# Kernel tuning notes

Measured on AMD Instinct MI355X. Metric: run time of the kernel, lower is better.

## Reference

```python
import jax, jax.numpy as jnp
import numpy as np

L, E, H, FF = 6, 768, 4, 3072
D = E // H
SCALE = float(E) ** -0.5  # note: source scales by embedding_size**-0.5, not head_dim
EPS = 1e-5


def layernorm(x, scale, bias):
    mu = jnp.mean(x, axis=-1, keepdims=True)
    var = jnp.mean((x - mu) ** 2, axis=-1, keepdims=True)
    return (x - mu) * jax.lax.rsqrt(var + EPS) * scale + bias


def setup_inputs() -> dict:
    key = jax.random.key(0)
    ks = jax.random.split(key, 16)
    s = 0.02
    inp = {
        "hidden_states": jax.random.normal(ks[0], (8, 1024, E), dtype=jnp.float32),
        "ln1_scale": jnp.ones((L, E), jnp.float32),
        "ln1_bias": jnp.zeros((L, E), jnp.float32),
        "wq": jax.random.normal(ks[1], (L, E, E), jnp.float32) * s,
        "wk": jax.random.normal(ks[2], (L, E, E), jnp.float32) * s,
        "wv": jax.random.normal(ks[3], (L, E, E), jnp.float32) * s,
        "wo": jax.random.normal(ks[4], (L, E, E), jnp.float32) * s,
        "bo": jnp.zeros((L, E), jnp.float32),
        "ln2_scale": jnp.ones((L, E), jnp.float32),
        "ln2_bias": jnp.zeros((L, E), jnp.float32),
        "w1": jax.random.normal(ks[5], (L, FF, E), jnp.float32) * s,
        "b1": jnp.zeros((L, FF), jnp.float32),
        "w2": jax.random.normal(ks[6], (L, E, FF), jnp.float32) * s,
        "b2": jnp.zeros((L, E), jnp.float32),
    }
    return inp


def _encoder(x, ln1_scale, ln1_bias, wq, wk, wv, wo, bo, ln2_scale, ln2_bias, w1, b1, w2, b2):
    B, S, _ = x.shape
    for i in range(L):
        h = layernorm(x, ln1_scale[i], ln1_bias[i])
        # torch Linear: y = x @ W.T
        q = (h @ wq[i].T).reshape(B, H, S, D)  # non-standard head split (reshape, no transpose) per source
        k = (h @ wk[i].T).reshape(B, H, S, D)
        v = (h @ wv[i].T).reshape(B, H, S, D)
        scores = jnp.einsum("bhsd,bhtd->bhst", q, k) * SCALE  # full SxS materialized, as in source
        attn = jax.nn.softmax(scores, axis=-1)
        o = jnp.einsum("bhst,bhtd->bhsd", attn, v)
        o = o.transpose(0, 2, 1, 3).reshape(B, S, E)
        x = x + (o @ wo[i].T + bo[i])
        h = layernorm(x, ln2_scale[i], ln2_bias[i])
        h = jax.nn.gelu(h @ w1[i].T + b1[i], approximate=False)  # nn.GELU default = exact erf
        x = x + (h @ w2[i].T + b2[i])  # dropout is identity in eval
    return x


def reference(hidden_states, ln1_scale, ln1_bias, wq, wk, wv, wo, bo, ln2_scale, ln2_bias, w1, b1, w2, b2):
    return _encoder(hidden_states, ln1_scale, ln1_bias, wq, wk, wv, wo, bo, ln2_scale, ln2_bias, w1, b1, w2, b2)
```

## Files before the change

kernel.cpp:

```cpp
#include <hip/hip_runtime.h>
#include <math.h>

typedef __attribute__((ext_vector_type(8))) __bf16 bf16x8;
typedef __attribute__((ext_vector_type(4))) __bf16 bf16x4;
typedef __attribute__((ext_vector_type(2))) __bf16 bf16x2;
typedef __attribute__((ext_vector_type(4))) float f32x4;

#define MFMA_BF16 __builtin_amdgcn_mfma_f32_16x16x32_bf16

constexpr int LAY = 6, E = 768, HH = 4, DH = 192, FF = 3072, BB = 8, SS = 1024, MM = 8192;
constexpr float ATT_SCALE = 0.03608439182435161f;

__device__ __forceinline__ void gl2lds16(const void* g, void* l) {
    __builtin_amdgcn_global_load_lds(
        (const __attribute__((address_space(1))) void*)g,
        (__attribute__((address_space(3))) void*)l, 16, 0, 0);
}

struct Cast6 {
    const float* src[6];
    __bf16* dst[6];
    int cum4[7];
};

__global__ __launch_bounds__(256) void cast6_kernel(Cast6 c, int total4) {
    int stride = gridDim.x * 256;
    for (int i = blockIdx.x * 256 + threadIdx.x; i < total4; i += stride) {
        int rgn = 0;
#pragma unroll
        for (int k = 1; k < 6; ++k) rgn += (i >= c.cum4[k]) ? 1 : 0;
        int off = i - c.cum4[rgn];
        f32x4 v = ((const f32x4*)c.src[rgn])[off];
        bf16x4 o;
        o[0] = (__bf16)v[0]; o[1] = (__bf16)v[1]; o[2] = (__bf16)v[2]; o[3] = (__bf16)v[3];
        ((bf16x4*)c.dst[rgn])[off] = o;
    }
}

__global__ __launch_bounds__(256) void ln_kernel(const float* __restrict__ x,
                                                 const float* __restrict__ gamma,
                                                 const float* __restrict__ beta,
                                                 __bf16* __restrict__ out) {
    size_t row = blockIdx.x;
    const float* xr = x + row * E;
    int t = threadIdx.x;
    float v0 = xr[t], v1 = xr[t + 256], v2 = xr[t + 512];
    float s = v0 + v1 + v2;
    float q = v0 * v0 + v1 * v1 + v2 * v2;
#pragma unroll
    for (int m = 1; m < 64; m <<= 1) { s += __shfl_xor(s, m); q += __shfl_xor(q, m); }
    __shared__ float red[8];
    int w = t >> 6;
    if ((t & 63) == 0) { red[w] = s; red[4 + w] = q; }
    __syncthreads();
    s = red[0] + red[1] + red[2] + red[3];
    q = red[4] + red[5] + red[6] + red[7];
    float mu = s * (1.0f / E);
    float var = q * (1.0f / E) - mu * mu;
    float rs = rsqrtf(var + 1e-5f);
    __bf16* orow = out + row * E;
    orow[t]       = (__bf16)((v0 - mu) * rs * gamma[t]       + beta[t]);
    orow[t + 256] = (__bf16)((v1 - mu) * rs * gamma[t + 256] + beta[t + 256]);
    orow[t + 512] = (__bf16)((v2 - mu) * rs * gamma[t + 512] + beta[t + 512]);
}

template <int EPI>
__global__ __launch_bounds__(256, 2) void gemm128(
    const __bf16* __restrict__ A,
    const __bf16* __restrict__ B0, const __bf16* __restrict__ B1, const __bf16* __restrict__ B2,
    void* __restrict__ O0, void* __restrict__ O1, void* __restrict__ O2,
    const float* __restrict__ bias, int M, int N, int K) {
    __shared__ __bf16 lds[4 * 8192];
    int z = blockIdx.z;
    const __bf16* Bw = (z == 0) ? B0 : (z == 1) ? B1 : B2;
    void* Out = (z == 0) ? O0 : (z == 1) ? O1 : O2;
    int t = threadIdx.x;
    int w = t >> 6, lane = t & 63, b4 = lane >> 4, r = lane & 15;
    int gx = gridDim.x;
    int nwg = gx * gridDim.y;
    int bid = blockIdx.y * gx + blockIdx.x;
    int cpx = nwg >> 3;
    int swz = (bid & 7) * cpx + (bid >> 3);
    int bx = swz % gx, by = swz / gx;
    int mbase = by * 128, nbase = bx * 128;
    int wr = w >> 1, wc = w & 1;
    const f32x4 fz = {0.f, 0.f, 0.f, 0.f};
    f32x4 acc[4][4];
#pragma unroll
    for (int a1 = 0; a1 < 4; ++a1)
#pragma unroll
        for (int a2 = 0; a2 < 4; ++a2) acc[a1][a2] = fz;
    const __bf16* Ap = A + (size_t)mbase * K;
    const __bf16* Bp = Bw + (size_t)nbase * K;
    int nk = K >> 5;

    auto stage = [&](const __bf16* P, int regionB, int tt) {
        int base = (tt & 3) * 8192 + regionB * 4096;
#pragma unroll
        for (int i = 0; i < 2; ++i) {
            int c = i * 256 + t;
            int row = c >> 2, cl = c & 3;
            int sc = cl ^ ((row >> 1) & 3);
            gl2lds16(P + (size_t)row * K + tt * 32 + sc * 8,
                     (void*)(lds + base + (i * 256 + w * 64) * 8));
        }
    };
    int swch = (b4 ^ ((r >> 1) & 3)) * 8;
    int aoff = (wr * 64 + r) * 32 + swch;
    int boff = 4096 + (wc * 64 + r) * 32 + swch;

    stage(Ap, 0, 0); stage(Bp, 1, 0); stage(Ap, 0, 1);
    stage(Bp, 1, 1); stage(Ap, 0, 2); stage(Bp, 1, 2);

    for (int tt = 0; tt < nk; ++tt) {
        if (tt < nk - 2)       asm volatile("s_waitcnt vmcnt(8)" ::: "memory");
        else if (tt == nk - 2) asm volatile("s_waitcnt vmcnt(4)" ::: "memory");
        else                   asm volatile("s_waitcnt vmcnt(0)" ::: "memory");
        __builtin_amdgcn_s_barrier();
        const __bf16* sa = lds + (tt & 3) * 8192;
        bool do_stage = (tt + 3) < nk;
        bf16x8 af[2], bfr[4];
#pragma unroll
        for (int ni = 0; ni < 4; ++ni) bfr[ni] = *(const bf16x8*)(sa + boff + ni * 512);
#pragma unroll
        for (int mi = 0; mi < 2; ++mi) af[mi] = *(const bf16x8*)(sa + aoff + mi * 512);
        if (do_stage) stage(Ap, 0, tt + 3);
        __builtin_amdgcn_s_setprio(1);
#pragma unroll
        for (int mi = 0; mi < 2; ++mi)
#pragma unroll
            for (int ni = 0; ni < 4; ++ni)
                acc[mi][ni] = MFMA_BF16(af[mi], bfr[ni], acc[mi][ni], 0, 0, 0);
        __builtin_amdgcn_s_setprio(0);
#pragma unroll
        for (int mi = 0; mi < 2; ++mi) af[mi] = *(const bf16x8*)(sa + aoff + (mi + 2) * 512);
        if (do_stage) stage(Bp, 1, tt + 3);
        __builtin_amdgcn_s_setprio(1);
#pragma unroll
        for (int mi = 0; mi < 2; ++mi)
#pragma unroll
            for (int ni = 0; ni < 4; ++ni)
                acc[mi + 2][ni] = MFMA_BF16(af[mi], bfr[ni], acc[mi + 2][ni], 0, 0, 0);
        __builtin_amdgcn_s_setprio(0);
    }

#pragma unroll
    for (int mi = 0; mi < 4; ++mi) {
#pragma unroll
        for (int ni = 0; ni < 4; ++ni) {
            int col = nbase + wc * 64 + ni * 16 + r;
#pragma unroll
            for (int j = 0; j < 4; ++j) {
                int rowi = mbase + wr * 64 + mi * 16 + b4 * 4 + j;
                float v = acc[mi][ni][j];
                if constexpr (EPI == 0) {
                    ((__bf16*)Out)[(size_t)rowi * N + col] = (__bf16)v;
                } else if constexpr (EPI == 1) {
                    v += bias[col];
                    float g = 0.5f * v * (1.0f + erff(v * 0.70710678118654752f));
                    ((__bf16*)Out)[(size_t)rowi * N + col] = (__bf16)g;
                } else {
                    float* X = (float*)Out;
                    X[(size_t)rowi * N + col] += v + bias[col];
                }
            }
        }
    }
}

__global__ __launch_bounds__(256) void vtrans_kernel(const __bf16* __restrict__ v,
                                                     __bf16* __restrict__ vt) {
    __shared__ __bf16 tile[64 * 72];
    int bh = blockIdx.y;
    int si = blockIdx.x / 3, di = blockIdx.x % 3;
    int t = threadIdx.x;
    const __bf16* src = v + (size_t)bh * (SS * DH) + (size_t)(si * 64) * DH + di * 64;
#pragma unroll
    for (int i = 0; i < 2; ++i) {
        int c = i * 256 + t;
        int sl = c >> 3, dc = c & 7;
        *(bf16x8*)(tile + sl * 72 + dc * 8) = *(const bf16x8*)(src + (size_t)sl * DH + dc * 8);
    }
    __syncthreads();
    __bf16* dst = vt + ((size_t)bh * DH + di * 64) * SS + si * 64;
#pragma unroll
    for (int i = 0; i < 2; ++i) {
        int c = i * 256 + t;
        int dl = c >> 3, sc = c & 7;
        bf16x8 o;
#pragma unroll
        for (int e = 0; e < 8; ++e) o[e] = tile[(sc * 8 + e) * 72 + dl];
        *(bf16x8*)(dst + (size_t)dl * SS + sc * 8) = o;
    }
}

__global__ __launch_bounds__(256) void attn_kernel(const __bf16* __restrict__ qp,
                                                   const __bf16* __restrict__ kp,
                                                   const __bf16* __restrict__ vtp,
                                                   __bf16* __restrict__ ao) {
    __shared__ __bf16 smK[64 * 192];
    __shared__ __bf16 smVt[192 * 64];
    __shared__ __bf16 smP[4 * 16 * 72];
    int qt = blockIdx.x, h = blockIdx.y, b = blockIdx.z;
    int t = threadIdx.x, w = t >> 6, lane = t & 63, b4 = lane >> 4, r = lane & 15;
    size_t base = (size_t)b * (SS * E) + (size_t)h * (SS * DH);
    const __bf16* Q = qp + base;
    const __bf16* Kg = kp + base;
    const __bf16* VtG = vtp + (size_t)(b * HH + h) * DH * SS;
    int q0 = qt * 64 + w * 16;
    bf16x8 qf[6];
#pragma unroll
    for (int ks = 0; ks < 6; ++ks)
        qf[ks] = *(const bf16x8*)(Q + (size_t)(q0 + r) * DH + ks * 32 + b4 * 8);
    const f32x4 fz = {0.f, 0.f, 0.f, 0.f};
    f32x4 oacc[12];
#pragma unroll
    for (int i = 0; i < 12; ++i) oacc[i] = fz;
    float m_r[4], l_r[4];
#pragma unroll
    for (int j = 0; j < 4; ++j) { m_r[j] = -1e30f; l_r[j] = 0.f; }
    __bf16* smPw = smP + w * (16 * 72);

    for (int kt = 0; kt < 16; ++kt) {
        const __bf16* Ks = Kg + (size_t)kt * 64 * DH;
#pragma unroll
        for (int i = 0; i < 6; ++i) {
            int c = i * 256 + t;
            int row = c / 24, cc = c - row * 24;
            int scc = (cc & 0x18) | ((cc ^ row) & 7);
            gl2lds16(Ks + (size_t)row * DH + scc * 8,
                     (void*)(smK + (i * 256 + w * 64) * 8));
        }
#pragma unroll
        for (int i = 0; i < 6; ++i) {
            int c = i * 256 + t;
            int row = c >> 3, cc = c & 7;
            int scc = cc ^ (row & 7);
            gl2lds16(VtG + (size_t)row * SS + kt * 64 + scc * 8,
                     (void*)(smVt + (i * 256 + w * 64) * 8));
        }
        __syncthreads();
        f32x4 sc[4];
#pragma unroll
        for (int nt = 0; nt < 4; ++nt) sc[nt] = fz;
#pragma unroll
        for (int ks = 0; ks < 6; ++ks) {
#pragma unroll
            for (int nt = 0; nt < 4; ++nt) {
                int cc = ks * 4 + b4;
                int ccs = (cc & 0x18) | ((cc ^ r) & 7);
                bf16x8 kf = *(const bf16x8*)(smK + (nt * 16 + r) * 192 + ccs * 8);
                sc[nt] = MFMA_BF16(qf[ks], kf, sc[nt], 0, 0, 0);
            }
        }
#pragma unroll
        for (int nt = 0; nt < 4; ++nt) sc[nt] *= ATT_SCALE;
        float alpha[4];
#pragma unroll
        for (int j = 0; j < 4; ++j) {
            float mx = fmaxf(fmaxf(sc[0][j], sc[1][j]), fmaxf(sc[2][j], sc[3][j]));
#pragma unroll
            for (int msk = 1; msk < 16; msk <<= 1) mx = fmaxf(mx, __shfl_xor(mx, msk));
            float mn = fmaxf(m_r[j], mx);
            alpha[j] = __expf(m_r[j] - mn);
            m_r[j] = mn;
            float p0 = __expf(sc[0][j] - mn);
            float p1 = __expf(sc[1][j] - mn);
            float p2 = __expf(sc[2][j] - mn);
            float p3 = __expf(sc[3][j] - mn);
            sc[0][j] = p0; sc[1][j] = p1; sc[2][j] = p2; sc[3][j] = p3;
            float ps = p0 + p1 + p2 + p3;
#pragma unroll
            for (int msk = 1; msk < 16; msk <<= 1) ps += __shfl_xor(ps, msk);
            l_r[j] = l_r[j] * alpha[j] + ps;
        }
        {
            f32x4 a4 = {alpha[0], alpha[1], alpha[2], alpha[3]};
#pragma unroll
            for (int i = 0; i < 12; ++i) oacc[i] *= a4;
        }
#pragma unroll
        for (int nt = 0; nt < 4; ++nt)
#pragma unroll
            for (int j = 0; j < 4; ++j)
                smPw[(b4 * 4 + j) * 72 + nt * 16 + r] = (__bf16)sc[nt][j];
        __asm__ volatile("s_waitcnt lgkmcnt(0)" ::: "memory");
#pragma unroll
        for (int kt2 = 0; kt2 < 2; ++kt2) {
            bf16x8 pa = *(const bf16x8*)(smPw + r * 72 + kt2 * 32 + b4 * 8);
#pragma unroll
            for (int nt = 0; nt < 12; ++nt) {
                int ccs = (kt2 * 4 + b4) ^ (r & 7);
                bf16x8 vf = *(const bf16x8*)(smVt + (nt * 16 + r) * 64 + ccs * 8);
                oacc[nt] = MFMA_BF16(pa, vf, oacc[nt], 0, 0, 0);
            }
        }
        __syncthreads();
    }
    float inv[4];
#pragma unroll
    for (int j = 0; j < 4; ++j) inv[j] = 1.0f / l_r[j];
    __bf16* obase = ao + (size_t)b * (SS * E);
#pragma unroll
    for (int nt = 0; nt < 12; ++nt)
#pragma unroll
        for (int j = 0; j < 4; ++j) {
            int srow = q0 + b4 * 4 + j;
            obase[(size_t)srow * E + h * DH + nt * 16 + r] = (__bf16)(oacc[nt][j] * inv[j]);
        }
}

extern "C" void kernel_launch(void* const* d_in, const int* in_sizes, int n_in,
                              void* d_out, int out_size, void* d_ws, size_t ws_size,
                              hipStream_t stream) {
    const float* hs   = (const float*)d_in[0];
    const float* ln1s = (const float*)d_in[1];
    const float* ln1b = (const float*)d_in[2];
    const float* wq   = (const float*)d_in[3];
    const float* wk   = (const float*)d_in[4];
    const float* wv   = (const float*)d_in[5];
    const float* wo   = (const float*)d_in[6];
    const float* bo   = (const float*)d_in[7];
    const float* ln2s = (const float*)d_in[8];
    const float* ln2b = (const float*)d_in[9];
    const float* w1   = (const float*)d_in[10];
    const float* b1   = (const float*)d_in[11];
    const float* w2   = (const float*)d_in[12];
    const float* b2   = (const float*)d_in[13];
    float* X = (float*)d_out;

    char* ws = (char*)d_ws;
    size_t off = 0;
    auto alloc = [&](size_t bytes) {
        char* p = ws + off;
        off += (bytes + 255) & ~(size_t)255;
        return p;
    };
    __bf16* wq_b = (__bf16*)alloc((size_t)E * E * 2);
    __bf16* wk_b = (__bf16*)alloc((size_t)E * E * 2);
    __bf16* wv_b = (__bf16*)alloc((size_t)E * E * 2);
    __bf16* wo_b = (__bf16*)alloc((size_t)E * E * 2);
    __bf16* w1_b = (__bf16*)alloc((size_t)FF * E * 2);
    __bf16* w2_b = (__bf16*)alloc((size_t)FF * E * 2);
    __bf16* h_b  = (__bf16*)alloc((size_t)MM * E * 2);
    char* U = alloc((size_t)MM * FF * 2);
    const size_t SLOT = (size_t)MM * E * 2;
    __bf16* q_b  = (__bf16*)U;
    __bf16* k_b  = (__bf16*)(U + SLOT);
    __bf16* v_b  = (__bf16*)(U + 2 * SLOT);
    __bf16* vt_b = (__bf16*)(U + 3 * SLOT);
    __bf16* a_b  = (__bf16*)(U + 2 * SLOT);
    __bf16* f_b  = (__bf16*)U;

    hipMemcpyAsync(d_out, hs, (size_t)MM * E * 4, hipMemcpyDeviceToDevice, stream);

    for (int i = 0; i < LAY; ++i) {
        Cast6 c;
        c.src[0] = wq + (size_t)i * E * E;  c.dst[0] = wq_b;
        c.src[1] = wk + (size_t)i * E * E;  c.dst[1] = wk_b;
        c.src[2] = wv + (size_t)i * E * E;  c.dst[2] = wv_b;
        c.src[3] = wo + (size_t)i * E * E;  c.dst[3] = wo_b;
        c.src[4] = w1 + (size_t)i * FF * E; c.dst[4] = w1_b;
        c.src[5] = w2 + (size_t)i * FF * E; c.dst[5] = w2_b;
        int n4[6] = {E * E / 4, E * E / 4, E * E / 4, E * E / 4, FF * E / 4, FF * E / 4};
        c.cum4[0] = 0;
        for (int k = 0; k < 6; ++k) c.cum4[k + 1] = c.cum4[k] + n4[k];
        int total4 = c.cum4[6];
        cast6_kernel<<<1024, 256, 0, stream>>>(c, total4);

        ln_kernel<<<MM, 256, 0, stream>>>(X, ln1s + (size_t)i * E, ln1b + (size_t)i * E, h_b);

        gemm128<0><<<dim3(E / 128, MM / 128, 3), 256, 0, stream>>>(
            h_b, wq_b, wk_b, wv_b, q_b, k_b, v_b, nullptr, MM, E, E);

        vtrans_kernel<<<dim3(48, 32), 256, 0, stream>>>(v_b, vt_b);

        attn_kernel<<<dim3(SS / 64, HH, BB), 256, 0, stream>>>(q_b, k_b, vt_b, a_b);

        gemm128<2><<<dim3(E / 128, MM / 128, 1), 256, 0, stream>>>(
            a_b, wo_b, wo_b, wo_b, X, X, X, bo + (size_t)i * E, MM, E, E);

        ln_kernel<<<MM, 256, 0, stream>>>(X, ln2s + (size_t)i * E, ln2b + (size_t)i * E, h_b);

        gemm128<1><<<dim3(FF / 128, MM / 128, 1), 256, 0, stream>>>(
            h_b, w1_b, w1_b, w1_b, f_b, f_b, f_b, b1 + (size_t)i * FF, MM, FF, E);

        gemm128<2><<<dim3(E / 128, MM / 128, 1), 256, 0, stream>>>(
            f_b, w2_b, w2_b, w2_b, X, X, X, b2 + (size_t)i * E, MM, E, FF);
    }
}
```

Measured before the change: 1.782 ms.

## Use 3-stage LDS pipeline, split-K with atomics for residual GEMMs

```diff
diff --git a/kernel.cpp b/kernel.cpp
--- a/kernel.cpp
+++ b/kernel.cpp
@@ -64,16 +64,25 @@
     orow[t + 512] = (__bf16)((v2 - mu) * rs * gamma[t + 512] + beta[t + 512]);
 }
 
-template <int EPI>
-__global__ __launch_bounds__(256, 2) void gemm128(
+template <int EPI, int SPLITK>
+__global__ __launch_bounds__(256, 3) void gemm128(
     const __bf16* __restrict__ A,
     const __bf16* __restrict__ B0, const __bf16* __restrict__ B1, const __bf16* __restrict__ B2,
     void* __restrict__ O0, void* __restrict__ O1, void* __restrict__ O2,
     const float* __restrict__ bias, int M, int N, int K) {
-    __shared__ __bf16 lds[4 * 8192];
+    __shared__ __bf16 lds[3 * 8192];
     int z = blockIdx.z;
-    const __bf16* Bw = (z == 0) ? B0 : (z == 1) ? B1 : B2;
-    void* Out = (z == 0) ? O0 : (z == 1) ? O1 : O2;
+    const __bf16* Bw;
+    void* Out;
+    int ksp;
+    if constexpr (SPLITK > 1) {
+        Bw = B0; Out = O0; ksp = z;
+    } else {
+        Bw = (z == 0) ? B0 : (z == 1) ? B1 : B2;
+        Out = (z == 0) ? O0 : (z == 1) ? O1 : O2;
+        ksp = 0;
+    }
+    int Keff = K / SPLITK;
     int t = threadIdx.x;
     int w = t >> 6, lane = t & 63, b4 = lane >> 4, r = lane & 15;
     int gx = gridDim.x;
@@ -90,41 +99,37 @@
     for (int a1 = 0; a1 < 4; ++a1)
 #pragma unroll
         for (int a2 = 0; a2 < 4; ++a2) acc[a1][a2] = fz;
-    const __bf16* Ap = A + (size_t)mbase * K;
-    const __bf16* Bp = Bw + (size_t)nbase * K;
-    int nk = K >> 5;
-
-    auto stage = [&](const __bf16* P, int regionB, int tt) {
-        int base = (tt & 3) * 8192 + regionB * 4096;
-#pragma unroll
-        for (int i = 0; i < 2; ++i) {
-            int c = i * 256 + t;
-            int row = c >> 2, cl = c & 3;
-            int sc = cl ^ ((row >> 1) & 3);
-            gl2lds16(P + (size_t)row * K + tt * 32 + sc * 8,
-                     (void*)(lds + base + (i * 256 + w * 64) * 8));
-        }
+    const __bf16* Ap = A + (size_t)mbase * K + ksp * Keff;
+    const __bf16* Bp = Bw + (size_t)nbase * K + ksp * Keff;
+    int nk = Keff >> 5;
+
+    int sc0 = ((t & 3) ^ ((t >> 3) & 3)) * 8;
+    const __bf16* pA0 = Ap + (size_t)(t >> 2) * K + sc0;
+    const __bf16* pA1 = pA0 + (size_t)64 * K;
+    const __bf16* pB0 = Bp + (size_t)(t >> 2) * K + sc0;
+    const __bf16* pB1 = pB0 + (size_t)64 * K;
+
+    auto stA = [&](int eoff, int slot) {
+        gl2lds16(pA0 + eoff, (void*)(lds + slot * 8192 + w * 512));
+        gl2lds16(pA1 + eoff, (void*)(lds + slot * 8192 + 2048 + w * 512));
     };
+    auto stB = [&](int eoff, int slot) {
+        gl2lds16(pB0 + eoff, (void*)(lds + slot * 8192 + 4096 + w * 512));
+        gl2lds16(pB1 + eoff, (void*)(lds + slot * 8192 + 6144 + w * 512));
+    };
+
     int swch = (b4 ^ ((r >> 1) & 3)) * 8;
     int aoff = (wr * 64 + r) * 32 + swch;
     int boff = 4096 + (wc * 64 + r) * 32 + swch;
 
-    stage(Ap, 0, 0); stage(Bp, 1, 0); stage(Ap, 0, 1);
-    stage(Bp, 1, 1); stage(Ap, 0, 2); stage(Bp, 1, 2);
-
-    for (int tt = 0; tt < nk; ++tt) {
-        if (tt < nk - 2)       asm volatile("s_waitcnt vmcnt(8)" ::: "memory");
-        else if (tt == nk - 2) asm volatile("s_waitcnt vmcnt(4)" ::: "memory");
-        else                   asm volatile("s_waitcnt vmcnt(0)" ::: "memory");
-        __builtin_amdgcn_s_barrier();
-        const __bf16* sa = lds + (tt & 3) * 8192;
-        bool do_stage = (tt + 3) < nk;
+    auto tile_body = [&](int p, int soff, int sslot, bool dost) {
+        const __bf16* sa = lds + p * 8192;
         bf16x8 af[2], bfr[4];
 #pragma unroll
         for (int ni = 0; ni < 4; ++ni) bfr[ni] = *(const bf16x8*)(sa + boff + ni * 512);
 #pragma unroll
         for (int mi = 0; mi < 2; ++mi) af[mi] = *(const bf16x8*)(sa + aoff + mi * 512);
-        if (do_stage) stage(Ap, 0, tt + 3);
+        if (dost) stA(soff, sslot);
         __builtin_amdgcn_s_setprio(1);
 #pragma unroll
         for (int mi = 0; mi < 2; ++mi)
@@ -134,7 +139,7 @@
         __builtin_amdgcn_s_setprio(0);
 #pragma unroll
         for (int mi = 0; mi < 2; ++mi) af[mi] = *(const bf16x8*)(sa + aoff + (mi + 2) * 512);
-        if (do_stage) stage(Bp, 1, tt + 3);
+        if (dost) stB(soff, sslot);
         __builtin_amdgcn_s_setprio(1);
 #pragma unroll
         for (int mi = 0; mi < 2; ++mi)
@@ -142,7 +147,28 @@
             for (int ni = 0; ni < 4; ++ni)
                 acc[mi + 2][ni] = MFMA_BF16(af[mi], bfr[ni], acc[mi + 2][ni], 0, 0, 0);
         __builtin_amdgcn_s_setprio(0);
-    }
+    };
+
+#define WAIT4 asm volatile("s_waitcnt vmcnt(4)" ::: "memory")
+#define WAIT0 asm volatile("s_waitcnt vmcnt(0)" ::: "memory")
+#define BAR   __builtin_amdgcn_s_barrier()
+
+    stA(0, 0); stB(0, 0); stA(32, 1); stB(32, 1);
+
+    int G = nk / 3;
+    for (int g = 0; g < G - 1; ++g) {
+        WAIT4; BAR; tile_body(0, 64, 2, true);
+        WAIT4; BAR; tile_body(1, 96, 0, true);
+        WAIT4; BAR; tile_body(2, 128, 1, true);
+        pA0 += 96; pA1 += 96; pB0 += 96; pB1 += 96;
+    }
+    WAIT4; BAR; tile_body(0, 64, 2, true);
+    WAIT4; BAR; tile_body(1, 0, 0, false);
+    WAIT0; BAR; tile_body(2, 0, 0, false);
+
+#undef WAIT4
+#undef WAIT0
+#undef BAR
 
 #pragma unroll
     for (int mi = 0; mi < 4; ++mi) {
@@ -161,7 +187,8 @@
                     ((__bf16*)Out)[(size_t)rowi * N + col] = (__bf16)g;
                 } else {
                     float* X = (float*)Out;
-                    X[(size_t)rowi * N + col] += v + bias[col];
+                    float add = v + (ksp == 0 ? bias[col] : 0.0f);
+                    atomicAdd(&X[(size_t)rowi * N + col], add);
                 }
             }
         }
@@ -370,22 +397,22 @@
 
         ln_kernel<<<MM, 256, 0, stream>>>(X, ln1s + (size_t)i * E, ln1b + (size_t)i * E, h_b);
 
-        gemm128<0><<<dim3(E / 128, MM / 128, 3), 256, 0, stream>>>(
+        gemm128<0, 1><<<dim3(E / 128, MM / 128, 3), 256, 0, stream>>>(
             h_b, wq_b, wk_b, wv_b, q_b, k_b, v_b, nullptr, MM, E, E);
 
         vtrans_kernel<<<dim3(48, 32), 256, 0, stream>>>(v_b, vt_b);
 
         attn_kernel<<<dim3(SS / 64, HH, BB), 256, 0, stream>>>(q_b, k_b, vt_b, a_b);
 
-        gemm128<2><<<dim3(E / 128, MM / 128, 1), 256, 0, stream>>>(
+        gemm128<2, 2><<<dim3(E / 128, MM / 128, 2), 256, 0, stream>>>(
             a_b, wo_b, wo_b, wo_b, X, X, X, bo + (size_t)i * E, MM, E, E);
 
         ln_kernel<<<MM, 256, 0, stream>>>(X, ln2s + (size_t)i * E, ln2b + (size_t)i * E, h_b);
 
-        gemm128<1><<<dim3(FF / 128, MM / 128, 1), 256, 0, stream>>>(
+        gemm128<1, 1><<<dim3(FF / 128, MM / 128, 1), 256, 0, stream>>>(
             h_b, w1_b, w1_b, w1_b, f_b, f_b, f_b, b1 + (size_t)i * FF, MM, FF, E);
 
-        gemm128<2><<<dim3(E / 128, MM / 128, 1), 256, 0, stream>>>(
+        gemm128<2, 2><<<dim3(E / 128, MM / 128, 2), 256, 0, stream>>>(
             f_b, w2_b, w2_b, w2_b, X, X, X, b2 + (size_t)i * E, MM, E, FF);
     }
 }
```

New measurement: 1.871 ms. 1.05x slower.
